# Optimization experiments

Measured on AMD Instinct MI355X. Metric: run time of the kernel, lower is better.

## Reference

```python
import jax, jax.numpy as jnp
import numpy as np

B, N, IN_DIM, OUT_DIM, H = 4, 2048, 1024, 1024, 16
HEAD_DIM = OUT_DIM // H  # 64


def setup_inputs() -> dict:
    key = jax.random.key(0)
    k_x, k_q, k_k, k_v, k_o = jax.random.split(key, 5)
    s = 1.0 / np.sqrt(IN_DIM)
    return {
        "x": jax.random.normal(k_x, (B, N, IN_DIM), dtype=jnp.float32),
        "w_q": jax.random.normal(k_q, (IN_DIM, OUT_DIM), dtype=jnp.float32) * s,
        "w_k": jax.random.normal(k_k, (IN_DIM, OUT_DIM), dtype=jnp.float32) * s,
        "w_v": jax.random.normal(k_v, (IN_DIM, OUT_DIM), dtype=jnp.float32) * s,
        "w_out": jax.random.normal(k_o, (OUT_DIM, OUT_DIM), dtype=jnp.float32) * s,
    }


def reference(x, w_q, w_k, w_v, w_out):
    b, n, _ = x.shape
    scale = 1.0 / jnp.sqrt(jnp.float32(HEAD_DIM))
    # QKV projections, split into heads: [b, h, n, d]
    q = (x @ w_q).reshape(b, n, H, HEAD_DIM).transpose(0, 2, 1, 3)
    k = (x @ w_k).reshape(b, n, H, HEAD_DIM).transpose(0, 2, 1, 3)
    v = (x @ w_v).reshape(b, n, H, HEAD_DIM).transpose(0, 2, 1, 3)
    # full score matrix [b, h, q, k]
    scores = jnp.einsum("bhqd,bhkd->bhqk", q, k) * scale
    # NOTE: source applies softmax over dim=1 (the HEAD axis) — reproduce exactly
    attn = jax.nn.softmax(scores, axis=1)
    # dropout p=0.0 -> identity
    ctx = jnp.einsum("bhqk,bhkd->bqhd", attn, v).reshape(b, n, OUT_DIM)
    return ctx @ w_out
```

## Files before the change

kernel.cpp:

```cpp
#include <hip/hip_runtime.h>
#include <hip/hip_bf16.h>

typedef unsigned short u16;
typedef unsigned int u32;
typedef __attribute__((ext_vector_type(8))) short short8;
typedef __attribute__((ext_vector_type(4))) float float4v;
typedef __attribute__((ext_vector_type(4))) unsigned int uint4v;

__device__ __forceinline__ u16 f2bf(float f) {
    union { float f; unsigned int u; } v; v.f = f;
    unsigned int r = v.u + 0x7fffu + ((v.u >> 16) & 1u);
    return (u16)(r >> 16);
}

__device__ __forceinline__ void gld_lds16(const u16* g, u16* l) {
    __builtin_amdgcn_global_load_lds(
        (const __attribute__((address_space(1))) u32*)g,
        (__attribute__((address_space(3))) u32*)l, 16, 0, 0);
}

__global__ __launch_bounds__(256) void convert_x(
    const float* __restrict__ x, u16* __restrict__ xb) {
    int i = (blockIdx.x * 256 + threadIdx.x) * 8;
    float4v a = *(const float4v*)&x[i];
    float4v b = *(const float4v*)&x[i + 4];
    u16 tmp[8] __attribute__((aligned(16)));
#pragma unroll
    for (int j = 0; j < 4; ++j) { tmp[j] = f2bf(a[j]); tmp[4 + j] = f2bf(b[j]); }
    *(uint4v*)&xb[i] = *(uint4v*)tmp;
}

__global__ __launch_bounds__(256) void transpose_w(
    const float* __restrict__ w0, const float* __restrict__ w1,
    const float* __restrict__ w2, const float* __restrict__ w3,
    u16* __restrict__ o0, u16* __restrict__ o1,
    u16* __restrict__ o2, u16* __restrict__ o3) {
    __shared__ u16 t[32][33];
    int z = blockIdx.z;
    const float* w = (z == 0) ? w0 : (z == 1) ? w1 : (z == 2) ? w2 : w3;
    u16* o         = (z == 0) ? o0 : (z == 1) ? o1 : (z == 2) ? o2 : o3;
    int bx = blockIdx.x * 32;
    int by = blockIdx.y * 32;
    int x = threadIdx.x, y = threadIdx.y;
#pragma unroll
    for (int i = 0; i < 4; ++i)
        t[y + i * 8][x] = f2bf(w[(size_t)(by + y + i * 8) * 1024 + bx + x]);
    __syncthreads();
#pragma unroll
    for (int i = 0; i < 4; ++i)
        o[(size_t)(bx + y + i * 8) * 1024 + by + x] = t[x][y + i * 8];
}

__global__ __launch_bounds__(256) void gemm_bt(
    const u16* __restrict__ A, const u16* __restrict__ Bt,
    void* __restrict__ Cout, int M, int N, int K, int mode) {
    __shared__ __attribute__((aligned(16))) u16 As[128 * 32];
    __shared__ __attribute__((aligned(16))) u16 Bs[128 * 32];
    const int tid = threadIdx.x;
    const int m0 = blockIdx.y * 128;
    const int n0 = blockIdx.x * 128;
    const int wid = tid >> 6;
    const int lane = tid & 63;
    const int ln = lane & 15, kq = lane >> 4;
    const int wm = (wid >> 1) * 64, wn = (wid & 1) * 64;

    float4v acc[4][4] = {};
    for (int k0 = 0; k0 < K; k0 += 32) {
#pragma unroll
        for (int i = 0; i < 2; ++i) {
            int chunk = tid + i * 256;
            int row = chunk >> 2, cg = chunk & 3;
            u16* lA = &As[(size_t)(i * 256 + wid * 64) * 8];
            u16* lB = &Bs[(size_t)(i * 256 + wid * 64) * 8];
            gld_lds16(&A[(size_t)(m0 + row) * K + k0 + cg * 8], lA);
            gld_lds16(&Bt[(size_t)(n0 + row) * K + k0 + cg * 8], lB);
        }
        __syncthreads();
        short8 af[4], bfr[4];
#pragma unroll
        for (int mt = 0; mt < 4; ++mt)
            af[mt] = *(const short8*)&As[(wm + mt * 16 + ln) * 32 + kq * 8];
#pragma unroll
        for (int nt = 0; nt < 4; ++nt)
            bfr[nt] = *(const short8*)&Bs[(wn + nt * 16 + ln) * 32 + kq * 8];
#pragma unroll
        for (int mt = 0; mt < 4; ++mt)
#pragma unroll
            for (int nt = 0; nt < 4; ++nt)
                acc[mt][nt] = __builtin_amdgcn_mfma_f32_16x16x32_bf16(
                    af[mt], bfr[nt], acc[mt][nt], 0, 0, 0);
        __syncthreads();
    }
    if (mode == 0) {
        u16* C = (u16*)Cout;
#pragma unroll
        for (int mt = 0; mt < 4; ++mt)
#pragma unroll
            for (int nt = 0; nt < 4; ++nt)
#pragma unroll
                for (int r = 0; r < 4; ++r) {
                    int row = m0 + wm + mt * 16 + kq * 4 + r;
                    int col = n0 + wn + nt * 16 + ln;
                    C[(size_t)row * N + col] = f2bf(acc[mt][nt][r]);
                }
    } else if (mode == 1) {
        u16* C = (u16*)Cout;
#pragma unroll
        for (int mt = 0; mt < 4; ++mt)
#pragma unroll
            for (int nt = 0; nt < 4; ++nt)
#pragma unroll
                for (int r = 0; r < 4; ++r) {
                    int t = m0 + wm + mt * 16 + kq * 4 + r;
                    int col = n0 + wn + nt * 16 + ln;
                    int b = t >> 11, n = t & 2047;
                    C[((size_t)(b * 1024 + col)) * 2048 + n] = f2bf(acc[mt][nt][r]);
                }
    } else {
        float* C = (float*)Cout;
#pragma unroll
        for (int mt = 0; mt < 4; ++mt)
#pragma unroll
            for (int nt = 0; nt < 4; ++nt)
#pragma unroll
                for (int r = 0; r < 4; ++r) {
                    int row = m0 + wm + mt * 16 + kq * 4 + r;
                    int col = n0 + wn + nt * 16 + ln;
                    C[(size_t)row * N + col] = acc[mt][nt][r];
                }
    }
}

__global__ __launch_bounds__(512, 2) void attn_kernel(
    const u16* qb, const u16* __restrict__ kb,
    const u16* __restrict__ vt, u16* cb) {
    __shared__ float E[16 * 32 * 36];
    __shared__ float Di[32 * 36];

    const int b = blockIdx.y;
    const int q0 = blockIdx.x * 32;
    const int tid = threadIdx.x;
    const int wid = tid >> 6, lane = tid & 63;
    const int ln = lane & 15, kq = lane >> 4;

    short8 aq[2][2][2];
#pragma unroll
    for (int hh = 0; hh < 2; ++hh) {
        int h = wid * 2 + hh;
#pragma unroll
        for (int mt = 0; mt < 2; ++mt)
#pragma unroll
            for (int kc = 0; kc < 2; ++kc)
                aq[hh][mt][kc] = *(const short8*)&qb[
                    (size_t)(b * 2048 + q0 + mt * 16 + ln) * 1024 +
                    h * 64 + kc * 32 + kq * 8];
    }
    float4v cacc[2][2][4] = {};

#pragma unroll 1
    for (int kt = 0; kt < 2048; kt += 32) {
        short8 bk[2][2][2];
        short8 bv[2][4];
#pragma unroll
        for (int hh = 0; hh < 2; ++hh) {
            int h = wid * 2 + hh;
#pragma unroll
            for (int kc = 0; kc < 2; ++kc)
#pragma unroll
                for (int nt = 0; nt < 2; ++nt)
                    bk[hh][kc][nt] = *(const short8*)&kb[
                        (size_t)(b * 2048 + kt + nt * 16 + ln) * 1024 +
                        h * 64 + kc * 32 + kq * 8];
        }
#pragma unroll
        for (int hh = 0; hh < 2; ++hh) {
            int h = wid * 2 + hh;
#pragma unroll
            for (int nt = 0; nt < 4; ++nt)
                bv[hh][nt] = *(const short8*)&vt[
                    (size_t)(b * 1024 + h * 64 + nt * 16 + ln) * 2048 + kt + kq * 8];
        }

        float4v sacc[2][2][2] = {};
#pragma unroll
        for (int hh = 0; hh < 2; ++hh)
#pragma unroll
            for (int kc = 0; kc < 2; ++kc)
#pragma unroll
                for (int mt = 0; mt < 2; ++mt)
#pragma unroll
                    for (int nt = 0; nt < 2; ++nt)
                        sacc[hh][mt][nt] = __builtin_amdgcn_mfma_f32_16x16x32_bf16(
                            aq[hh][mt][kc], bk[hh][kc][nt], sacc[hh][mt][nt], 0, 0, 0);
        __syncthreads();
#pragma unroll
        for (int hh = 0; hh < 2; ++hh) {
            int h = wid * 2 + hh;
#pragma unroll
            for (int mt = 0; mt < 2; ++mt)
#pragma unroll
                for (int nt = 0; nt < 2; ++nt)
#pragma unroll
                    for (int r = 0; r < 4; ++r) {
                        float s = sacc[hh][mt][nt][r] * 0.125f;
                        E[(h * 32 + mt * 16 + kq * 4 + r) * 36 + nt * 16 + ln] =
                            __expf(fminf(s, 80.0f));
                    }
        }
        __syncthreads();

#pragma unroll
        for (int i = 0; i < 2; ++i) {
            int p = tid + i * 512;
            int q = p >> 5, kk = p & 31;
            float d = 0.f;
#pragma unroll
            for (int h = 0; h < 16; ++h)
                d += E[(h * 32 + q) * 36 + kk];
            Di[q * 36 + kk] = __builtin_amdgcn_rcpf(d);
        }
        __syncthreads();

#pragma unroll
        for (int hh = 0; hh < 2; ++hh) {
            int h = wid * 2 + hh;
            short8 ap[2];
#pragma unroll
            for (int mt = 0; mt < 2; ++mt) {
                const float* ep = &E[(h * 32 + mt * 16 + ln) * 36 + kq * 8];
                const float* dp = &Di[(mt * 16 + ln) * 36 + kq * 8];
                u16 tmp[8] __attribute__((aligned(16)));
#pragma unroll
                for (int j = 0; j < 8; ++j)
                    tmp[j] = f2bf(ep[j] * dp[j]);
                ap[mt] = *(short8*)tmp;
            }
#pragma unroll
            for (int nt = 0; nt < 4; ++nt)
#pragma unroll
                for (int mt = 0; mt < 2; ++mt)
                    cacc[hh][mt][nt] = __builtin_amdgcn_mfma_f32_16x16x32_bf16(
                        ap[mt], bv[hh][nt], cacc[hh][mt][nt], 0, 0, 0);
        }
    }

#pragma unroll
    for (int hh = 0; hh < 2; ++hh) {
        int h = wid * 2 + hh;
#pragma unroll
        for (int mt = 0; mt < 2; ++mt)
#pragma unroll
            for (int nt = 0; nt < 4; ++nt)
#pragma unroll
                for (int r = 0; r < 4; ++r) {
                    int row = b * 2048 + q0 + mt * 16 + kq * 4 + r;
                    int col = h * 64 + nt * 16 + ln;
                    cb[(size_t)row * 1024 + col] = f2bf(cacc[hh][mt][nt][r]);
                }
    }
}

extern "C" void kernel_launch(void* const* d_in, const int* in_sizes, int n_in,
                              void* d_out, int out_size, void* d_ws, size_t ws_size,
                              hipStream_t stream) {
    const float* x   = (const float*)d_in[0];
    const float* w_q = (const float*)d_in[1];
    const float* w_k = (const float*)d_in[2];
    const float* w_v = (const float*)d_in[3];
    const float* w_o = (const float*)d_in[4];

    char* ws = (char*)d_ws;
    const size_t SZ_W   = (size_t)1024 * 1024 * 2;
    const size_t SZ_TOK = (size_t)8192 * 1024 * 2;
    u16* x_bf  = (u16*)(ws);
    u16* wtq   = (u16*)(ws + SZ_TOK);
    u16* wtk   = (u16*)(ws + SZ_TOK + SZ_W);
    u16* wtv   = (u16*)(ws + SZ_TOK + 2 * SZ_W);
    u16* wto   = (u16*)(ws + SZ_TOK + 3 * SZ_W);
    u16* q_buf = (u16*)(ws + SZ_TOK + 4 * SZ_W);
    u16* k_buf  = (u16*)d_out;
    u16* vt_buf = (u16*)d_out + (size_t)8192 * 1024;

    convert_x<<<4096, 256, 0, stream>>>(x, x_bf);

    transpose_w<<<dim3(32, 32, 4), dim3(32, 8), 0, stream>>>(
        w_q, w_k, w_v, w_o, wtq, wtk, wtv, wto);

    gemm_bt<<<dim3(8, 64), 256, 0, stream>>>(x_bf, wtq, q_buf, 8192, 1024, 1024, 0);
    gemm_bt<<<dim3(8, 64), 256, 0, stream>>>(x_bf, wtk, k_buf, 8192, 1024, 1024, 0);
    gemm_bt<<<dim3(8, 64), 256, 0, stream>>>(x_bf, wtv, vt_buf, 8192, 1024, 1024, 1);

    attn_kernel<<<dim3(64, 4), 512, 0, stream>>>(q_buf, k_buf, vt_buf, q_buf);

    gemm_bt<<<dim3(8, 64), 256, 0, stream>>>(q_buf, wto, d_out, 8192, 1024, 1024, 2);
}
```

Measured before the change: 516.6 us.

## Use one wave per head and double-buffered bf16 exp tile in attention

The attention kernel now launches 1024 threads so each of the 16 waves owns a single head instead of two. The exponentiated scores are stored as bf16 in a double-buffered shared tile, which removes one barrier per key tile and halves LDS traffic. exp2f with a pre-scaled constant replaces __expf. In exchange, exp values are rounded to bf16 before the head-sum normalisation, which costs precision, and fewer blocks fit per CU.

```diff
diff --git a/kernel.cpp b/kernel.cpp
--- a/kernel.cpp
+++ b/kernel.cpp
@@ -11,6 +11,10 @@
     union { float f; unsigned int u; } v; v.f = f;
     unsigned int r = v.u + 0x7fffu + ((v.u >> 16) & 1u);
     return (u16)(r >> 16);
+}
+__device__ __forceinline__ float bf2f(u16 h) {
+    union { unsigned int u; float f; } v; v.u = ((unsigned int)h) << 16;
+    return v.f;
 }
 
 __device__ __forceinline__ void gld_lds16(const u16* g, u16* l) {
@@ -131,10 +135,10 @@
     }
 }
 
-__global__ __launch_bounds__(512, 2) void attn_kernel(
+__global__ __launch_bounds__(1024) void attn_kernel(
     const u16* qb, const u16* __restrict__ kb,
     const u16* __restrict__ vt, u16* cb) {
-    __shared__ float E[16 * 32 * 36];
+    __shared__ __attribute__((aligned(16))) u16 E[2][16 * 32 * 40];
     __shared__ float Di[32 * 36];
 
     const int b = blockIdx.y;
@@ -142,122 +146,97 @@
     const int tid = threadIdx.x;
     const int wid = tid >> 6, lane = tid & 63;
     const int ln = lane & 15, kq = lane >> 4;
-
-    short8 aq[2][2][2];
-#pragma unroll
-    for (int hh = 0; hh < 2; ++hh) {
-        int h = wid * 2 + hh;
-#pragma unroll
-        for (int mt = 0; mt < 2; ++mt)
-#pragma unroll
-            for (int kc = 0; kc < 2; ++kc)
-                aq[hh][mt][kc] = *(const short8*)&qb[
-                    (size_t)(b * 2048 + q0 + mt * 16 + ln) * 1024 +
-                    h * 64 + kc * 32 + kq * 8];
-    }
-    float4v cacc[2][2][4] = {};
+    const int h = wid;
+
+    short8 aq[2][2];
+#pragma unroll
+    for (int mt = 0; mt < 2; ++mt)
+#pragma unroll
+        for (int kc = 0; kc < 2; ++kc)
+            aq[mt][kc] = *(const short8*)&qb[
+                (size_t)(b * 2048 + q0 + mt * 16 + ln) * 1024 +
+                h * 64 + kc * 32 + kq * 8];
+
+    float4v cacc[2][4] = {};
 
 #pragma unroll 1
     for (int kt = 0; kt < 2048; kt += 32) {
-        short8 bk[2][2][2];
-        short8 bv[2][4];
-#pragma unroll
-        for (int hh = 0; hh < 2; ++hh) {
-            int h = wid * 2 + hh;
-#pragma unroll
-            for (int kc = 0; kc < 2; ++kc)
+        const int cur = (kt >> 5) & 1;
+        short8 bk[2][2];
+        short8 bv[4];
+#pragma unroll
+        for (int kc = 0; kc < 2; ++kc)
+#pragma unroll
+            for (int nt = 0; nt < 2; ++nt)
+                bk[kc][nt] = *(const short8*)&kb[
+                    (size_t)(b * 2048 + kt + nt * 16 + ln) * 1024 +
+                    h * 64 + kc * 32 + kq * 8];
+#pragma unroll
+        for (int nt = 0; nt < 4; ++nt)
+            bv[nt] = *(const short8*)&vt[
+                (size_t)(b * 1024 + h * 64 + nt * 16 + ln) * 2048 + kt + kq * 8];
+
+        float4v sacc[2][2] = {};
+#pragma unroll
+        for (int kc = 0; kc < 2; ++kc)
+#pragma unroll
+            for (int mt = 0; mt < 2; ++mt)
 #pragma unroll
                 for (int nt = 0; nt < 2; ++nt)
-                    bk[hh][kc][nt] = *(const short8*)&kb[
-                        (size_t)(b * 2048 + kt + nt * 16 + ln) * 1024 +
-                        h * 64 + kc * 32 + kq * 8];
-        }
-#pragma unroll
-        for (int hh = 0; hh < 2; ++hh) {
-            int h = wid * 2 + hh;
-#pragma unroll
-            for (int nt = 0; nt < 4; ++nt)
-                bv[hh][nt] = *(const short8*)&vt[
-                    (size_t)(b * 1024 + h * 64 + nt * 16 + ln) * 2048 + kt + kq * 8];
-        }
-
-        float4v sacc[2][2][2] = {};
-#pragma unroll
-        for (int hh = 0; hh < 2; ++hh)
-#pragma unroll
-            for (int kc = 0; kc < 2; ++kc)
-#pragma unroll
-                for (int mt = 0; mt < 2; ++mt)
-#pragma unroll
-                    for (int nt = 0; nt < 2; ++nt)
-                        sacc[hh][mt][nt] = __builtin_amdgcn_mfma_f32_16x16x32_bf16(
-                            aq[hh][mt][kc], bk[hh][kc][nt], sacc[hh][mt][nt], 0, 0, 0);
-        __syncthreads();
-#pragma unroll
-        for (int hh = 0; hh < 2; ++hh) {
-            int h = wid * 2 + hh;
-#pragma unroll
-            for (int mt = 0; mt < 2; ++mt)
-#pragma unroll
-                for (int nt = 0; nt < 2; ++nt)
-#pragma unroll
-                    for (int r = 0; r < 4; ++r) {
-                        float s = sacc[hh][mt][nt][r] * 0.125f;
-                        E[(h * 32 + mt * 16 + kq * 4 + r) * 36 + nt * 16 + ln] =
-                            __expf(fminf(s, 80.0f));
-                    }
-        }
-        __syncthreads();
-
-#pragma unroll
-        for (int i = 0; i < 2; ++i) {
-            int p = tid + i * 512;
-            int q = p >> 5, kk = p & 31;
+                    sacc[mt][nt] = __builtin_amdgcn_mfma_f32_16x16x32_bf16(
+                        aq[mt][kc], bk[kc][nt], sacc[mt][nt], 0, 0, 0);
+
+#pragma unroll
+        for (int mt = 0; mt < 2; ++mt)
+#pragma unroll
+            for (int nt = 0; nt < 2; ++nt)
+#pragma unroll
+                for (int r = 0; r < 4; ++r) {
+                    float s = sacc[mt][nt][r] * 0.18033688f;
+                    E[cur][(h * 32 + mt * 16 + kq * 4 + r) * 40 + nt * 16 + ln] =
+                        f2bf(exp2f(fminf(s, 115.0f)));
+                }
+        __syncthreads();
+
+        {
+            int q = tid >> 5, kk = tid & 31;
             float d = 0.f;
 #pragma unroll
-            for (int h = 0; h < 16; ++h)
-                d += E[(h * 32 + q) * 36 + kk];
+            for (int hh = 0; hh < 16; ++hh)
+                d += bf2f(E[cur][(hh * 32 + q) * 40 + kk]);
             Di[q * 36 + kk] = __builtin_amdgcn_rcpf(d);
         }
         __syncthreads();
 
-#pragma unroll
-        for (int hh = 0; hh < 2; ++hh) {
-            int h = wid * 2 + hh;
-            short8 ap[2];
-#pragma unroll
-            for (int mt = 0; mt < 2; ++mt) {
-                const float* ep = &E[(h * 32 + mt * 16 + ln) * 36 + kq * 8];
-                const float* dp = &Di[(mt * 16 + ln) * 36 + kq * 8];
-                u16 tmp[8] __attribute__((aligned(16)));
-#pragma unroll
-                for (int j = 0; j < 8; ++j)
-                    tmp[j] = f2bf(ep[j] * dp[j]);
-                ap[mt] = *(short8*)tmp;
+        short8 ap[2];
+#pragma unroll
+        for (int mt = 0; mt < 2; ++mt) {
+            const u16* ep = &E[cur][(h * 32 + mt * 16 + ln) * 40 + kq * 8];
+            const float* dp = &Di[(mt * 16 + ln) * 36 + kq * 8];
+            u16 tmp[8] __attribute__((aligned(16)));
+#pragma unroll
+            for (int j = 0; j < 8; ++j)
+                tmp[j] = f2bf(bf2f(ep[j]) * dp[j]);
+            ap[mt] = *(short8*)tmp;
+        }
+#pragma unroll
+        for (int nt = 0; nt < 4; ++nt)
+#pragma unroll
+            for (int mt = 0; mt < 2; ++mt)
+                cacc[mt][nt] = __builtin_amdgcn_mfma_f32_16x16x32_bf16(
+                    ap[mt], bv[nt], cacc[mt][nt], 0, 0, 0);
+    }
+
+#pragma unroll
+    for (int mt = 0; mt < 2; ++mt)
+#pragma unroll
+        for (int nt = 0; nt < 4; ++nt)
+#pragma unroll
+            for (int r = 0; r < 4; ++r) {
+                int row = b * 2048 + q0 + mt * 16 + kq * 4 + r;
+                int col = h * 64 + nt * 16 + ln;
+                cb[(size_t)row * 1024 + col] = f2bf(cacc[mt][nt][r]);
             }
-#pragma unroll
-            for (int nt = 0; nt < 4; ++nt)
-#pragma unroll
-                for (int mt = 0; mt < 2; ++mt)
-                    cacc[hh][mt][nt] = __builtin_amdgcn_mfma_f32_16x16x32_bf16(
-                        ap[mt], bv[hh][nt], cacc[hh][mt][nt], 0, 0, 0);
-        }
-    }
-
-#pragma unroll
-    for (int hh = 0; hh < 2; ++hh) {
-        int h = wid * 2 + hh;
-#pragma unroll
-        for (int mt = 0; mt < 2; ++mt)
-#pragma unroll
-            for (int nt = 0; nt < 4; ++nt)
-#pragma unroll
-                for (int r = 0; r < 4; ++r) {
-                    int row = b * 2048 + q0 + mt * 16 + kq * 4 + r;
-                    int col = h * 64 + nt * 16 + ln;
-                    cb[(size_t)row * 1024 + col] = f2bf(cacc[hh][mt][nt][r]);
-                }
-    }
 }
 
 extern "C" void kernel_launch(void* const* d_in, const int* in_sizes, int n_in,
@@ -290,7 +269,7 @@
     gemm_bt<<<dim3(8, 64), 256, 0, stream>>>(x_bf, wtk, k_buf, 8192, 1024, 1024, 0);
     gemm_bt<<<dim3(8, 64), 256, 0, stream>>>(x_bf, wtv, vt_buf, 8192, 1024, 1024, 1);
 
-    attn_kernel<<<dim3(64, 4), 512, 0, stream>>>(q_buf, k_buf, vt_buf, q_buf);
+    attn_kernel<<<dim3(64, 4), 1024, 0, stream>>>(q_buf, k_buf, vt_buf, q_buf);
 
     gemm_bt<<<dim3(8, 64), 256, 0, stream>>>(q_buf, wto, d_out, 8192, 1024, 1024, 2);
 }
```

New measurement: 509.2 us. About the same (-1.4%).
